# Kernel optimization log

Measured on AMD Instinct MI355X. Metric: run time of the kernel, lower is better.

The kernel has to match this reference:

```python
import jax, jax.numpy as jnp
import numpy as np

B, N, FIN = 4, 4096, 128
H, U = 4, 32

def setup_inputs() -> dict:
    key = jax.random.key(0)
    k = jax.random.split(key, 6)
    x = jax.random.normal(k[0], (B, N, FIN), dtype=jnp.float32)
    adj = (jax.random.uniform(k[1], (B, N, N)) < 0.05).astype(jnp.float32)
    glorot = lambda kk, shape, fi, fo: jax.random.uniform(kk, shape, jnp.float32,
                                                          -np.sqrt(6.0/(fi+fo)), np.sqrt(6.0/(fi+fo)))
    W = glorot(k[2], (FIN, H*U), FIN, H*U)
    a_src = glorot(k[3], (H, U, 1), U, 1)
    a_dst = glorot(k[4], (H, U, 1), U, 1)
    bias = jnp.zeros((H*U,), dtype=jnp.float32)
    return {"x": x, "adj": adj, "W": W, "a_src": a_src, "a_dst": a_dst, "bias": bias}

def reference(x, adj, W, a_src, a_dst, bias):
    # inference mode: attention dropout is a no-op
    b, n, _ = x.shape
    h_heads, u = a_src.shape[0], a_src.shape[1]
    # add self-loops, clip to {0,1}
    adj = jnp.clip(adj + jnp.eye(n, dtype=adj.dtype)[None], 0.0, 1.0)
    h = (x @ W).reshape(b, n, h_heads, u).transpose(0, 2, 1, 3)      # [B,H,N,U]
    f1 = jnp.einsum('bhnu,hu->bhn', h, a_src[..., 0])                # [B,H,N]
    f2 = jnp.einsum('bhnu,hu->bhn', h, a_dst[..., 0])                # [B,H,N]
    e = f1[:, :, :, None] + f2[:, :, None, :]                        # [B,H,N,N]
    e = jnp.where(e > 0, e, 0.2 * e)                                 # LeakyReLU(0.2)
    e = jnp.where(adj[:, None] > 0.0, e, jnp.float32(-1e9))
    alpha = jax.nn.softmax(e, axis=-1)
    out = jnp.einsum('bhij,bhju->bhiu', alpha, h)                    # [B,H,N,U]
    out = out.transpose(0, 2, 1, 3).reshape(b, n, h_heads * u) + bias
    return jnp.where(out > 0, out, jnp.expm1(out))                   # ELU
```

## Files before the change

### kernel.cpp

```cpp
#include <hip/hip_runtime.h>
#include <math.h>

#define NB   4
#define NN   4096
#define FIN  128
#define FOUT 128
#define NH   4
#define UU   32

__device__ __forceinline__ unsigned short f2bf(float f) {
    unsigned u = __float_as_uint(f);
    u += 0x7fff + ((u >> 16) & 1);
    return (unsigned short)(u >> 16);
}

#define LBAR() asm volatile("s_waitcnt lgkmcnt(0)\n\ts_barrier" ::: "memory")

#define K1_ROWS 64
#define K1_RT   8
#define K1_CT   4
#define XPAD    132

__global__ __launch_bounds__(256) void k1_feat(
    const float* __restrict__ x, const float* __restrict__ W,
    const float* __restrict__ a_src, const float* __restrict__ a_dst,
    unsigned short* __restrict__ hbf, float* __restrict__ f1g, float* __restrict__ f2g)
{
    __shared__ __align__(16) float Wq[32 * FOUT];
    __shared__ __align__(16) float xs[K1_ROWS * XPAD];

    const int tid  = threadIdx.x;
    const int row0 = blockIdx.x * K1_ROWS;

    const float4* x4 = (const float4*)(x + (size_t)row0 * FIN);
    for (int idx = tid; idx < K1_ROWS * FIN / 4; idx += 256) {
        int r = idx >> 5, q = idx & 31;
        *(float4*)(xs + r * XPAD + q * 4) = x4[idx];
    }

    const int cg = tid & 31;
    const int rg = tid >> 5;
    float acc[K1_RT][K1_CT];
    #pragma unroll
    for (int rr = 0; rr < K1_RT; rr++)
        #pragma unroll
        for (int cc = 0; cc < K1_CT; cc++) acc[rr][cc] = 0.f;

    for (int kt = 0; kt < 4; kt++) {
        __syncthreads();
        for (int idx = tid; idx < 32 * FOUT / 4; idx += 256)
            ((float4*)Wq)[idx] = ((const float4*)W)[kt * 1024 + idx];
        __syncthreads();
        #pragma unroll
        for (int k4 = 0; k4 < 8; k4++) {
            const int kb = kt * 32 + k4 * 4;
            float4 xv[K1_RT];
            #pragma unroll
            for (int rr = 0; rr < K1_RT; rr++)
                xv[rr] = *(const float4*)(xs + (rg * K1_RT + rr) * XPAD + kb);
            #pragma unroll
            for (int kk = 0; kk < 4; kk++) {
                float wv[K1_CT];
                #pragma unroll
                for (int cc = 0; cc < K1_CT; cc++)
                    wv[cc] = Wq[(k4 * 4 + kk) * FOUT + cg + 32 * cc];
                #pragma unroll
                for (int rr = 0; rr < K1_RT; rr++) {
                    float xk = ((const float*)&xv[rr])[kk];
                    #pragma unroll
                    for (int cc = 0; cc < K1_CT; cc++)
                        acc[rr][cc] = fmaf(xk, wv[cc], acc[rr][cc]);
                }
            }
        }
    }
    __syncthreads();
    #pragma unroll
    for (int rr = 0; rr < K1_RT; rr++)
        #pragma unroll
        for (int cc = 0; cc < K1_CT; cc++)
            xs[(rg * K1_RT + rr) * XPAD + cg + 32 * cc] = acc[rr][cc];
    __syncthreads();

    unsigned short* hrow = hbf + (size_t)row0 * FOUT;
    for (int idx = tid; idx < K1_ROWS * FOUT / 8; idx += 256) {
        int r = idx >> 4, q = idx & 15;
        const float* src = xs + r * XPAD + q * 8;
        uint4 o;
        o.x = (unsigned)f2bf(src[0]) | ((unsigned)f2bf(src[1]) << 16);
        o.y = (unsigned)f2bf(src[2]) | ((unsigned)f2bf(src[3]) << 16);
        o.z = (unsigned)f2bf(src[4]) | ((unsigned)f2bf(src[5]) << 16);
        o.w = (unsigned)f2bf(src[6]) | ((unsigned)f2bf(src[7]) << 16);
        *(uint4*)(hrow + (size_t)r * FOUT + q * 8) = o;
    }

    for (int task = tid; task < K1_ROWS * NH * 2; task += 256) {
        int row = task >> 3;
        int head = (task >> 1) & 3;
        int which = task & 1;
        const float* av = which ? a_dst : a_src;
        float s = 0.f;
        #pragma unroll
        for (int u = 0; u < UU; u++)
            s += xs[row * XPAD + head * UU + u] * av[head * UU + u];
        float* dst = which ? f2g : f1g;
        dst[(size_t)(row0 + row) * NH + head] = s;
    }
}

#define CAP   512
#define PPART 132
#define RPB   8

__device__ __forceinline__ float lrelu(float e) { return e > 0.f ? e : 0.2f * e; }

__global__ __launch_bounds__(256, 4) void k2_gat(
    const float* __restrict__ adj, const unsigned short* __restrict__ hbf,
    const float* __restrict__ f1g, const float* __restrict__ f2g,
    const float* __restrict__ bias, float* __restrict__ out)
{
    const int p    = blockIdx.x;
    const int xcd  = p & 7;
    const int b    = xcd >> 1;
    const int l    = ((p >> 3) << 1) | (p & 1);
    const int tid  = threadIdx.x;
    const int lane = tid & 63;
    const int wv   = tid >> 6;

    __shared__ int    nbr[CAP];
    __shared__ __align__(16) float4 alpha4[CAP];
    __shared__ float  part[16][PPART];
    __shared__ __align__(16) float4 smax4[4];
    __shared__ float  wsum[16];
    __shared__ int    wcnt[4];

    const float4* f2b = (const float4*)(f2g + (size_t)b * NN * NH);
    const unsigned short* hbase = hbf + (size_t)b * NN * FOUT;
    const unsigned long long below = (1ull << lane) - 1ull;

    const int cq = tid & 15, kg = tid >> 4, hh = cq >> 2;
    const unsigned short* hb = hbase + cq * 8;
    const float bias_r = (tid < FOUT) ? bias[tid] : 0.f;

    int i = l;
    float4 v[4], vn[4], f1v, f1n;
    {
        const float4* arow = (const float4*)(adj + (size_t)(b * NN + i) * NN);
        #pragma unroll
        for (int it = 0; it < 4; it++) v[it] = arow[wv * 256 + it * 64 + lane];
        f1v = ((const float4*)f1g)[b * NN + i];
    }

    for (int t = 0; t < RPB; t++) {
        const int row = b * NN + i;

        int my_cnt = 0;
        #pragma unroll
        for (int it = 0; it < 4; it++) {
            const int jb = (wv * 256 + it * 64 + lane) << 2;
            my_cnt += __popcll(__ballot((v[it].x > 0.f) | (jb + 0 == i)));
            my_cnt += __popcll(__ballot((v[it].y > 0.f) | (jb + 1 == i)));
            my_cnt += __popcll(__ballot((v[it].z > 0.f) | (jb + 2 == i)));
            my_cnt += __popcll(__ballot((v[it].w > 0.f) | (jb + 3 == i)));
        }
        if (lane == 0) wcnt[wv] = my_cnt;
        LBAR();

        const int w0 = wcnt[0], w1 = wcnt[1], w2 = wcnt[2], w3 = wcnt[3];
        int run = (wv > 0 ? w0 : 0) + (wv > 1 ? w1 : 0) + (wv > 2 ? w2 : 0);
        const int total = w0 + w1 + w2 + w3;
        const int K = (total < CAP) ? total : CAP;

        #pragma unroll
        for (int it = 0; it < 4; it++) {
            const int jb = (wv * 256 + it * 64 + lane) << 2;
            const bool p0 = (v[it].x > 0.f) | (jb + 0 == i);
            const bool p1 = (v[it].y > 0.f) | (jb + 1 == i);
            const bool p2 = (v[it].z > 0.f) | (jb + 2 == i);
            const bool p3 = (v[it].w > 0.f) | (jb + 3 == i);
            unsigned long long m0 = __ballot(p0), m1 = __ballot(p1);
            unsigned long long m2 = __ballot(p2), m3 = __ballot(p3);
            int c0 = __popcll(m0), c1 = __popcll(m1), c2 = __popcll(m2), c3 = __popcll(m3);
            if (p0) { int s = run + __popcll(m0 & below);                if (s < CAP) nbr[s] = jb + 0; }
            if (p1) { int s = run + c0 + __popcll(m1 & below);           if (s < CAP) nbr[s] = jb + 1; }
            if (p2) { int s = run + c0 + c1 + __popcll(m2 & below);      if (s < CAP) nbr[s] = jb + 2; }
            if (p3) { int s = run + c0 + c1 + c2 + __popcll(m3 & below); if (s < CAP) nbr[s] = jb + 3; }
            run += c0 + c1 + c2 + c3;
        }

        if (t + 1 < RPB) {
            const int inext = i + 512;
            const float4* arowN = (const float4*)(adj + (size_t)(b * NN + inext) * NN);
            #pragma unroll
            for (int it = 0; it < 4; it++) vn[it] = arowN[wv * 256 + it * 64 + lane];
            f1n = ((const float4*)f1g)[b * NN + inext];
        }
        LBAR();

        float4 hmax = make_float4(-1e30f, -1e30f, -1e30f, -1e30f);
        for (int k = tid; k < K; k += 256) {
            int j = nbr[k];
            float4 f2v = f2b[j];
            float4 e;
            e.x = lrelu(f1v.x + f2v.x);
            e.y = lrelu(f1v.y + f2v.y);
            e.z = lrelu(f1v.z + f2v.z);
            e.w = lrelu(f1v.w + f2v.w);
            alpha4[k] = e;
            hmax.x = fmaxf(hmax.x, e.x); hmax.y = fmaxf(hmax.y, e.y);
            hmax.z = fmaxf(hmax.z, e.z); hmax.w = fmaxf(hmax.w, e.w);
        }
        #pragma unroll
        for (int off = 32; off > 0; off >>= 1) {
            hmax.x = fmaxf(hmax.x, __shfl_xor(hmax.x, off, 64));
            hmax.y = fmaxf(hmax.y, __shfl_xor(hmax.y, off, 64));
            hmax.z = fmaxf(hmax.z, __shfl_xor(hmax.z, off, 64));
            hmax.w = fmaxf(hmax.w, __shfl_xor(hmax.w, off, 64));
        }
        if (lane == 0) smax4[wv] = hmax;
        LBAR();

        float4 g0 = smax4[0], g1 = smax4[1], g2 = smax4[2], g3 = smax4[3];
        float4 gmax;
        gmax.x = fmaxf(fmaxf(g0.x, g1.x), fmaxf(g2.x, g3.x));
        gmax.y = fmaxf(fmaxf(g0.y, g1.y), fmaxf(g2.y, g3.y));
        gmax.z = fmaxf(fmaxf(g0.z, g1.z), fmaxf(g2.z, g3.z));
        gmax.w = fmaxf(fmaxf(g0.w, g1.w), fmaxf(g2.w, g3.w));
        float4 hsum = make_float4(0.f, 0.f, 0.f, 0.f);
        for (int k = tid; k < K; k += 256) {
            float4 e = alpha4[k];
            e.x = __expf(e.x - gmax.x);
            e.y = __expf(e.y - gmax.y);
            e.z = __expf(e.z - gmax.z);
            e.w = __expf(e.w - gmax.w);
            alpha4[k] = e;
            hsum.x += e.x; hsum.y += e.y; hsum.z += e.z; hsum.w += e.w;
        }
        #pragma unroll
        for (int off = 32; off > 0; off >>= 1) {
            hsum.x += __shfl_xor(hsum.x, off, 64);
            hsum.y += __shfl_xor(hsum.y, off, 64);
            hsum.z += __shfl_xor(hsum.z, off, 64);
            hsum.w += __shfl_xor(hsum.w, off, 64);
        }
        if (lane == 0) {
            wsum[wv * 4 + 0] = hsum.x; wsum[wv * 4 + 1] = hsum.y;
            wsum[wv * 4 + 2] = hsum.z; wsum[wv * 4 + 3] = hsum.w;
        }
        LBAR();

        const float* alpf = (const float*)alpha4;
        float acc[8];
        #pragma unroll
        for (int u = 0; u < 8; u++) acc[u] = 0.f;
        int k = kg;
        for (; k + 16 < K; k += 32) {
            int j0 = nbr[k], j1 = nbr[k + 16];
            float a0 = alpf[k * 4 + hh], a1 = alpf[(k + 16) * 4 + hh];
            uint4 u4a = *(const uint4*)(hb + (size_t)j0 * FOUT);
            uint4 u4b = *(const uint4*)(hb + (size_t)j1 * FOUT);
            const unsigned* u0 = (const unsigned*)&u4a;
            const unsigned* u1 = (const unsigned*)&u4b;
            #pragma unroll
            for (int u = 0; u < 4; u++) {
                acc[2*u]   = fmaf(a0, __uint_as_float(u0[u] << 16),         acc[2*u]);
                acc[2*u+1] = fmaf(a0, __uint_as_float(u0[u] & 0xffff0000u), acc[2*u+1]);
            }
            #pragma unroll
            for (int u = 0; u < 4; u++) {
                acc[2*u]   = fmaf(a1, __uint_as_float(u1[u] << 16),         acc[2*u]);
                acc[2*u+1] = fmaf(a1, __uint_as_float(u1[u] & 0xffff0000u), acc[2*u+1]);
            }
        }
        if (k < K) {
            int j0 = nbr[k];
            float a0 = alpf[k * 4 + hh];
            uint4 u4a = *(const uint4*)(hb + (size_t)j0 * FOUT);
            const unsigned* u0 = (const unsigned*)&u4a;
            #pragma unroll
            for (int u = 0; u < 4; u++) {
                acc[2*u]   = fmaf(a0, __uint_as_float(u0[u] << 16),         acc[2*u]);
                acc[2*u+1] = fmaf(a0, __uint_as_float(u0[u] & 0xffff0000u), acc[2*u+1]);
            }
        }
        *(float4*)&part[kg][cq * 8]     = *(float4*)&acc[0];
        *(float4*)&part[kg][cq * 8 + 4] = *(float4*)&acc[4];
        LBAR();

        if (tid < FOUT) {
            const int h = tid >> 5;
            float s = wsum[h] + wsum[4 + h] + wsum[8 + h] + wsum[12 + h];
            float o = 0.f;
            #pragma unroll
            for (int g = 0; g < 16; g++) o += part[g][tid];
            o = o / s + bias_r;
            o = o > 0.f ? o : expm1f(o);
            out[(size_t)row * FOUT + tid] = o;
        }
        LBAR();

        if (t + 1 < RPB) {
            #pragma unroll
            for (int it = 0; it < 4; it++) v[it] = vn[it];
            f1v = f1n;
            i += 512;
        }
    }
}

extern "C" void kernel_launch(void* const* d_in, const int* in_sizes, int n_in,
                              void* d_out, int out_size, void* d_ws, size_t ws_size,
                              hipStream_t stream) {
    const float* x     = (const float*)d_in[0];
    const float* adj   = (const float*)d_in[1];
    const float* W     = (const float*)d_in[2];
    const float* a_src = (const float*)d_in[3];
    const float* a_dst = (const float*)d_in[4];
    const float* bias  = (const float*)d_in[5];
    float* out = (float*)d_out;

    char* ws = (char*)d_ws;
    unsigned short* hbf = (unsigned short*)ws;
    float* f1g = (float*)(ws + (size_t)NB * NN * FOUT * 2);
    float* f2g = f1g + (size_t)NB * NN * NH;

    k1_feat<<<NB * NN / K1_ROWS, 256, 0, stream>>>(x, W, a_src, a_dst, hbf, f1g, f2g);
    k2_gat<<<NB * NN / RPB, 256, 0, stream>>>(adj, hbf, f1g, f2g, bias, out);
}
```

Measured before the change: 437.4 us.

## Move adjacency compaction into the feature kernel and run one row per block

Neighbor-list extraction from the dense adjacency now runs in extra blocks of the first kernel, one wavefront per row. Each row's compacted 16-bit index list and count go to workspace, so the adjacency streaming overlaps the x@W projection. The attention kernel then reads the compact list and processes a single row per block with 16384 blocks. The cost is an extra global write and read of the neighbor lists, and the loss of the prefetch pipelining that previously hid adjacency loads behind compute.

```diff
diff --git a/kernel.cpp b/kernel.cpp
--- a/kernel.cpp
+++ b/kernel.cpp
@@ -7,6 +7,7 @@
 #define FOUT 128
 #define NH   4
 #define UU   32
+#define CAP  512
 
 __device__ __forceinline__ unsigned short f2bf(float f) {
     unsigned u = __float_as_uint(f);
@@ -16,20 +17,59 @@
 
 #define LBAR() asm volatile("s_waitcnt lgkmcnt(0)\n\ts_barrier" ::: "memory")
 
+__device__ __forceinline__ float lrelu(float e) { return e > 0.f ? e : 0.2f * e; }
+
 #define K1_ROWS 64
 #define K1_RT   8
 #define K1_CT   4
 #define XPAD    132
-
-__global__ __launch_bounds__(256) void k1_feat(
+#define K1_BLOCKS 256
+
+__global__ __launch_bounds__(256) void k0_fused(
     const float* __restrict__ x, const float* __restrict__ W,
     const float* __restrict__ a_src, const float* __restrict__ a_dst,
-    unsigned short* __restrict__ hbf, float* __restrict__ f1g, float* __restrict__ f2g)
+    const float* __restrict__ adj,
+    unsigned short* __restrict__ hbf, float* __restrict__ f1g, float* __restrict__ f2g,
+    unsigned short* __restrict__ nbr_g, int* __restrict__ kcnt)
 {
+    const int tid  = threadIdx.x;
+    const int lane = tid & 63;
+    const int wv   = tid >> 6;
+
     __shared__ __align__(16) float Wq[32 * FOUT];
     __shared__ __align__(16) float xs[K1_ROWS * XPAD];
 
-    const int tid  = threadIdx.x;
+    if (blockIdx.x >= K1_BLOCKS) {
+        const int r = (blockIdx.x - K1_BLOCKS) * 4 + wv;
+        const int i = r & (NN - 1);
+        const float4* arow = (const float4*)(adj + (size_t)r * NN);
+        float4 v[16];
+        #pragma unroll
+        for (int it = 0; it < 16; it++) v[it] = arow[it * 64 + lane];
+
+        unsigned short* ng = nbr_g + (size_t)r * CAP;
+        const unsigned long long below = (1ull << lane) - 1ull;
+        int run = 0;
+        #pragma unroll
+        for (int it = 0; it < 16; it++) {
+            const int jb = (it * 64 + lane) << 2;
+            const bool p0 = (v[it].x > 0.f) | (jb + 0 == i);
+            const bool p1 = (v[it].y > 0.f) | (jb + 1 == i);
+            const bool p2 = (v[it].z > 0.f) | (jb + 2 == i);
+            const bool p3 = (v[it].w > 0.f) | (jb + 3 == i);
+            unsigned long long m0 = __ballot(p0), m1 = __ballot(p1);
+            unsigned long long m2 = __ballot(p2), m3 = __ballot(p3);
+            int c0 = __popcll(m0), c1 = __popcll(m1), c2 = __popcll(m2), c3 = __popcll(m3);
+            if (p0) { int s = run + __popcll(m0 & below);                if (s < CAP) ng[s] = (unsigned short)(jb + 0); }
+            if (p1) { int s = run + c0 + __popcll(m1 & below);           if (s < CAP) ng[s] = (unsigned short)(jb + 1); }
+            if (p2) { int s = run + c0 + c1 + __popcll(m2 & below);      if (s < CAP) ng[s] = (unsigned short)(jb + 2); }
+            if (p3) { int s = run + c0 + c1 + c2 + __popcll(m3 & below); if (s < CAP) ng[s] = (unsigned short)(jb + 3); }
+            run += c0 + c1 + c2 + c3;
+        }
+        if (lane == 0) kcnt[r] = (run < CAP) ? run : CAP;
+        return;
+    }
+
     const int row0 = blockIdx.x * K1_ROWS;
 
     const float4* x4 = (const float4*)(x + (size_t)row0 * FIN);
@@ -60,16 +100,16 @@
                 xv[rr] = *(const float4*)(xs + (rg * K1_RT + rr) * XPAD + kb);
             #pragma unroll
             for (int kk = 0; kk < 4; kk++) {
-                float wv[K1_CT];
+                float wvv[K1_CT];
                 #pragma unroll
                 for (int cc = 0; cc < K1_CT; cc++)
-                    wv[cc] = Wq[(k4 * 4 + kk) * FOUT + cg + 32 * cc];
+                    wvv[cc] = Wq[(k4 * 4 + kk) * FOUT + cg + 32 * cc];
                 #pragma unroll
                 for (int rr = 0; rr < K1_RT; rr++) {
                     float xk = ((const float*)&xv[rr])[kk];
                     #pragma unroll
                     for (int cc = 0; cc < K1_CT; cc++)
-                        acc[rr][cc] = fmaf(xk, wv[cc], acc[rr][cc]);
+                        acc[rr][cc] = fmaf(xk, wvv[cc], acc[rr][cc]);
                 }
             }
         }
@@ -108,21 +148,19 @@
     }
 }
 
-#define CAP   512
 #define PPART 132
-#define RPB   8
-
-__device__ __forceinline__ float lrelu(float e) { return e > 0.f ? e : 0.2f * e; }
-
-__global__ __launch_bounds__(256, 4) void k2_gat(
-    const float* __restrict__ adj, const unsigned short* __restrict__ hbf,
+
+__global__ __launch_bounds__(256) void k2_gat(
+    const unsigned short* __restrict__ nbr_g, const int* __restrict__ kcnt,
+    const unsigned short* __restrict__ hbf,
     const float* __restrict__ f1g, const float* __restrict__ f2g,
     const float* __restrict__ bias, float* __restrict__ out)
 {
-    const int p    = blockIdx.x;
-    const int xcd  = p & 7;
+    const int q    = blockIdx.x;
+    const int xcd  = q & 7;
     const int b    = xcd >> 1;
-    const int l    = ((p >> 3) << 1) | (p & 1);
+    const int i    = ((q >> 3) << 1) | (q & 1);
+    const int row  = b * NN + i;
     const int tid  = threadIdx.x;
     const int lane = tid & 63;
     const int wv   = tid >> 6;
@@ -132,179 +170,117 @@
     __shared__ float  part[16][PPART];
     __shared__ __align__(16) float4 smax4[4];
     __shared__ float  wsum[16];
-    __shared__ int    wcnt[4];
+
+    const int K = kcnt[row];
+
+    const unsigned short* ng = nbr_g + (size_t)row * CAP;
+    for (int k = tid; k < K; k += 256) nbr[k] = (int)ng[k];
+    LBAR();
 
     const float4* f2b = (const float4*)(f2g + (size_t)b * NN * NH);
-    const unsigned short* hbase = hbf + (size_t)b * NN * FOUT;
-    const unsigned long long below = (1ull << lane) - 1ull;
+    const float4  f1v = ((const float4*)f1g)[row];
+
+    float4 hmax = make_float4(-1e30f, -1e30f, -1e30f, -1e30f);
+    for (int k = tid; k < K; k += 256) {
+        int j = nbr[k];
+        float4 f2v = f2b[j];
+        float4 e;
+        e.x = lrelu(f1v.x + f2v.x);
+        e.y = lrelu(f1v.y + f2v.y);
+        e.z = lrelu(f1v.z + f2v.z);
+        e.w = lrelu(f1v.w + f2v.w);
+        alpha4[k] = e;
+        hmax.x = fmaxf(hmax.x, e.x); hmax.y = fmaxf(hmax.y, e.y);
+        hmax.z = fmaxf(hmax.z, e.z); hmax.w = fmaxf(hmax.w, e.w);
+    }
+    #pragma unroll
+    for (int off = 32; off > 0; off >>= 1) {
+        hmax.x = fmaxf(hmax.x, __shfl_xor(hmax.x, off, 64));
+        hmax.y = fmaxf(hmax.y, __shfl_xor(hmax.y, off, 64));
+        hmax.z = fmaxf(hmax.z, __shfl_xor(hmax.z, off, 64));
+        hmax.w = fmaxf(hmax.w, __shfl_xor(hmax.w, off, 64));
+    }
+    if (lane == 0) smax4[wv] = hmax;
+    LBAR();
+
+    float4 g0 = smax4[0], g1 = smax4[1], g2 = smax4[2], g3 = smax4[3];
+    float4 gmax;
+    gmax.x = fmaxf(fmaxf(g0.x, g1.x), fmaxf(g2.x, g3.x));
+    gmax.y = fmaxf(fmaxf(g0.y, g1.y), fmaxf(g2.y, g3.y));
+    gmax.z = fmaxf(fmaxf(g0.z, g1.z), fmaxf(g2.z, g3.z));
+    gmax.w = fmaxf(fmaxf(g0.w, g1.w), fmaxf(g2.w, g3.w));
+    float4 hsum = make_float4(0.f, 0.f, 0.f, 0.f);
+    for (int k = tid; k < K; k += 256) {
+        float4 e = alpha4[k];
+        e.x = __expf(e.x - gmax.x);
+        e.y = __expf(e.y - gmax.y);
+        e.z = __expf(e.z - gmax.z);
+        e.w = __expf(e.w - gmax.w);
+        alpha4[k] = e;
+        hsum.x += e.x; hsum.y += e.y; hsum.z += e.z; hsum.w += e.w;
+    }
+    #pragma unroll
+    for (int off = 32; off > 0; off >>= 1) {
+        hsum.x += __shfl_xor(hsum.x, off, 64);
+        hsum.y += __shfl_xor(hsum.y, off, 64);
+        hsum.z += __shfl_xor(hsum.z, off, 64);
+        hsum.w += __shfl_xor(hsum.w, off, 64);
+    }
+    if (lane == 0) {
+        wsum[wv * 4 + 0] = hsum.x; wsum[wv * 4 + 1] = hsum.y;
+        wsum[wv * 4 + 2] = hsum.z; wsum[wv * 4 + 3] = hsum.w;
+    }
+    LBAR();
 
     const int cq = tid & 15, kg = tid >> 4, hh = cq >> 2;
-    const unsigned short* hb = hbase + cq * 8;
-    const float bias_r = (tid < FOUT) ? bias[tid] : 0.f;
-
-    int i = l;
-    float4 v[4], vn[4], f1v, f1n;
-    {
-        const float4* arow = (const float4*)(adj + (size_t)(b * NN + i) * NN);
-        #pragma unroll
-        for (int it = 0; it < 4; it++) v[it] = arow[wv * 256 + it * 64 + lane];
-        f1v = ((const float4*)f1g)[b * NN + i];
-    }
-
-    for (int t = 0; t < RPB; t++) {
-        const int row = b * NN + i;
-
-        int my_cnt = 0;
-        #pragma unroll
-        for (int it = 0; it < 4; it++) {
-            const int jb = (wv * 256 + it * 64 + lane) << 2;
-            my_cnt += __popcll(__ballot((v[it].x > 0.f) | (jb + 0 == i)));
-            my_cnt += __popcll(__ballot((v[it].y > 0.f) | (jb + 1 == i)));
-            my_cnt += __popcll(__ballot((v[it].z > 0.f) | (jb + 2 == i)));
-            my_cnt += __popcll(__ballot((v[it].w > 0.f) | (jb + 3 == i)));
-        }
-        if (lane == 0) wcnt[wv] = my_cnt;
-        LBAR();
-
-        const int w0 = wcnt[0], w1 = wcnt[1], w2 = wcnt[2], w3 = wcnt[3];
-        int run = (wv > 0 ? w0 : 0) + (wv > 1 ? w1 : 0) + (wv > 2 ? w2 : 0);
-        const int total = w0 + w1 + w2 + w3;
-        const int K = (total < CAP) ? total : CAP;
-
-        #pragma unroll
-        for (int it = 0; it < 4; it++) {
-            const int jb = (wv * 256 + it * 64 + lane) << 2;
-            const bool p0 = (v[it].x > 0.f) | (jb + 0 == i);
-            const bool p1 = (v[it].y > 0.f) | (jb + 1 == i);
-            const bool p2 = (v[it].z > 0.f) | (jb + 2 == i);
-            const bool p3 = (v[it].w > 0.f) | (jb + 3 == i);
-            unsigned long long m0 = __ballot(p0), m1 = __ballot(p1);
-            unsigned long long m2 = __ballot(p2), m3 = __ballot(p3);
-            int c0 = __popcll(m0), c1 = __popcll(m1), c2 = __popcll(m2), c3 = __popcll(m3);
-            if (p0) { int s = run + __popcll(m0 & below);                if (s < CAP) nbr[s] = jb + 0; }
-            if (p1) { int s = run + c0 + __popcll(m1 & below);           if (s < CAP) nbr[s] = jb + 1; }
-            if (p2) { int s = run + c0 + c1 + __popcll(m2 & below);      if (s < CAP) nbr[s] = jb + 2; }
-            if (p3) { int s = run + c0 + c1 + c2 + __popcll(m3 & below); if (s < CAP) nbr[s] = jb + 3; }
-            run += c0 + c1 + c2 + c3;
-        }
-
-        if (t + 1 < RPB) {
-            const int inext = i + 512;
-            const float4* arowN = (const float4*)(adj + (size_t)(b * NN + inext) * NN);
-            #pragma unroll
-            for (int it = 0; it < 4; it++) vn[it] = arowN[wv * 256 + it * 64 + lane];
-            f1n = ((const float4*)f1g)[b * NN + inext];
-        }
-        LBAR();
-
-        float4 hmax = make_float4(-1e30f, -1e30f, -1e30f, -1e30f);
-        for (int k = tid; k < K; k += 256) {
-            int j = nbr[k];
-            float4 f2v = f2b[j];
-            float4 e;
-            e.x = lrelu(f1v.x + f2v.x);
-            e.y = lrelu(f1v.y + f2v.y);
-            e.z = lrelu(f1v.z + f2v.z);
-            e.w = lrelu(f1v.w + f2v.w);
-            alpha4[k] = e;
-            hmax.x = fmaxf(hmax.x, e.x); hmax.y = fmaxf(hmax.y, e.y);
-            hmax.z = fmaxf(hmax.z, e.z); hmax.w = fmaxf(hmax.w, e.w);
-        }
-        #pragma unroll
-        for (int off = 32; off > 0; off >>= 1) {
-            hmax.x = fmaxf(hmax.x, __shfl_xor(hmax.x, off, 64));
-            hmax.y = fmaxf(hmax.y, __shfl_xor(hmax.y, off, 64));
-            hmax.z = fmaxf(hmax.z, __shfl_xor(hmax.z, off, 64));
-            hmax.w = fmaxf(hmax.w, __shfl_xor(hmax.w, off, 64));
-        }
-        if (lane == 0) smax4[wv] = hmax;
-        LBAR();
-
-        float4 g0 = smax4[0], g1 = smax4[1], g2 = smax4[2], g3 = smax4[3];
-        float4 gmax;
-        gmax.x = fmaxf(fmaxf(g0.x, g1.x), fmaxf(g2.x, g3.x));
-        gmax.y = fmaxf(fmaxf(g0.y, g1.y), fmaxf(g2.y, g3.y));
-        gmax.z = fmaxf(fmaxf(g0.z, g1.z), fmaxf(g2.z, g3.z));
-        gmax.w = fmaxf(fmaxf(g0.w, g1.w), fmaxf(g2.w, g3.w));
-        float4 hsum = make_float4(0.f, 0.f, 0.f, 0.f);
-        for (int k = tid; k < K; k += 256) {
-            float4 e = alpha4[k];
-            e.x = __expf(e.x - gmax.x);
-            e.y = __expf(e.y - gmax.y);
-            e.z = __expf(e.z - gmax.z);
-            e.w = __expf(e.w - gmax.w);
-            alpha4[k] = e;
-            hsum.x += e.x; hsum.y += e.y; hsum.z += e.z; hsum.w += e.w;
-        }
-        #pragma unroll
-        for (int off = 32; off > 0; off >>= 1) {
-            hsum.x += __shfl_xor(hsum.x, off, 64);
-            hsum.y += __shfl_xor(hsum.y, off, 64);
-            hsum.z += __shfl_xor(hsum.z, off, 64);
-            hsum.w += __shfl_xor(hsum.w, off, 64);
-        }
-        if (lane == 0) {
-            wsum[wv * 4 + 0] = hsum.x; wsum[wv * 4 + 1] = hsum.y;
-            wsum[wv * 4 + 2] = hsum.z; wsum[wv * 4 + 3] = hsum.w;
-        }
-        LBAR();
-
-        const float* alpf = (const float*)alpha4;
-        float acc[8];
-        #pragma unroll
-        for (int u = 0; u < 8; u++) acc[u] = 0.f;
-        int k = kg;
-        for (; k + 16 < K; k += 32) {
-            int j0 = nbr[k], j1 = nbr[k + 16];
-            float a0 = alpf[k * 4 + hh], a1 = alpf[(k + 16) * 4 + hh];
-            uint4 u4a = *(const uint4*)(hb + (size_t)j0 * FOUT);
-            uint4 u4b = *(const uint4*)(hb + (size_t)j1 * FOUT);
-            const unsigned* u0 = (const unsigned*)&u4a;
-            const unsigned* u1 = (const unsigned*)&u4b;
-            #pragma unroll
-            for (int u = 0; u < 4; u++) {
-                acc[2*u]   = fmaf(a0, __uint_as_float(u0[u] << 16),         acc[2*u]);
-                acc[2*u+1] = fmaf(a0, __uint_as_float(u0[u] & 0xffff0000u), acc[2*u+1]);
-            }
-            #pragma unroll
-            for (int u = 0; u < 4; u++) {
-                acc[2*u]   = fmaf(a1, __uint_as_float(u1[u] << 16),         acc[2*u]);
-                acc[2*u+1] = fmaf(a1, __uint_as_float(u1[u] & 0xffff0000u), acc[2*u+1]);
-            }
-        }
-        if (k < K) {
-            int j0 = nbr[k];
-            float a0 = alpf[k * 4 + hh];
-            uint4 u4a = *(const uint4*)(hb + (size_t)j0 * FOUT);
-            const unsigned* u0 = (const unsigned*)&u4a;
-            #pragma unroll
-            for (int u = 0; u < 4; u++) {
-                acc[2*u]   = fmaf(a0, __uint_as_float(u0[u] << 16),         acc[2*u]);
-                acc[2*u+1] = fmaf(a0, __uint_as_float(u0[u] & 0xffff0000u), acc[2*u+1]);
-            }
-        }
-        *(float4*)&part[kg][cq * 8]     = *(float4*)&acc[0];
-        *(float4*)&part[kg][cq * 8 + 4] = *(float4*)&acc[4];
-        LBAR();
-
-        if (tid < FOUT) {
-            const int h = tid >> 5;
-            float s = wsum[h] + wsum[4 + h] + wsum[8 + h] + wsum[12 + h];
-            float o = 0.f;
-            #pragma unroll
-            for (int g = 0; g < 16; g++) o += part[g][tid];
-            o = o / s + bias_r;
-            o = o > 0.f ? o : expm1f(o);
-            out[(size_t)row * FOUT + tid] = o;
-        }
-        LBAR();
-
-        if (t + 1 < RPB) {
-            #pragma unroll
-            for (int it = 0; it < 4; it++) v[it] = vn[it];
-            f1v = f1n;
-            i += 512;
-        }
+    const unsigned short* hb = hbf + (size_t)b * NN * FOUT + cq * 8;
+    const float* alpf = (const float*)alpha4;
+    float acc[8];
+    #pragma unroll
+    for (int u = 0; u < 8; u++) acc[u] = 0.f;
+    int k = kg;
+    for (; k + 16 < K; k += 32) {
+        int j0 = nbr[k], j1 = nbr[k + 16];
+        float a0 = alpf[k * 4 + hh], a1 = alpf[(k + 16) * 4 + hh];
+        uint4 u4a = *(const uint4*)(hb + (size_t)j0 * FOUT);
+        uint4 u4b = *(const uint4*)(hb + (size_t)j1 * FOUT);
+        const unsigned* u0 = (const unsigned*)&u4a;
+        const unsigned* u1 = (const unsigned*)&u4b;
+        #pragma unroll
+        for (int u = 0; u < 4; u++) {
+            acc[2*u]   = fmaf(a0, __uint_as_float(u0[u] << 16),         acc[2*u]);
+            acc[2*u+1] = fmaf(a0, __uint_as_float(u0[u] & 0xffff0000u), acc[2*u+1]);
+        }
+        #pragma unroll
+        for (int u = 0; u < 4; u++) {
+            acc[2*u]   = fmaf(a1, __uint_as_float(u1[u] << 16),         acc[2*u]);
+            acc[2*u+1] = fmaf(a1, __uint_as_float(u1[u] & 0xffff0000u), acc[2*u+1]);
+        }
+    }
+    if (k < K) {
+        int j0 = nbr[k];
+        float a0 = alpf[k * 4 + hh];
+        uint4 u4a = *(const uint4*)(hb + (size_t)j0 * FOUT);
+        const unsigned* u0 = (const unsigned*)&u4a;
+        #pragma unroll
+        for (int u = 0; u < 4; u++) {
+            acc[2*u]   = fmaf(a0, __uint_as_float(u0[u] << 16),         acc[2*u]);
+            acc[2*u+1] = fmaf(a0, __uint_as_float(u0[u] & 0xffff0000u), acc[2*u+1]);
+        }
+    }
+    *(float4*)&part[kg][cq * 8]     = *(float4*)&acc[0];
+    *(float4*)&part[kg][cq * 8 + 4] = *(float4*)&acc[4];
+    LBAR();
+
+    if (tid < FOUT) {
+        const int h = tid >> 5;
+        float s = wsum[h] + wsum[4 + h] + wsum[8 + h] + wsum[12 + h];
+        float o = 0.f;
+        #pragma unroll
+        for (int g = 0; g < 16; g++) o += part[g][tid];
+        o = o / s + bias[tid];
+        o = o > 0.f ? o : expm1f(o);
+        out[(size_t)row * FOUT + tid] = o;
     }
 }
 
@@ -320,10 +296,13 @@
     float* out = (float*)d_out;
 
     char* ws = (char*)d_ws;
-    unsigned short* hbf = (unsigned short*)ws;
-    float* f1g = (float*)(ws + (size_t)NB * NN * FOUT * 2);
-    float* f2g = f1g + (size_t)NB * NN * NH;
-
-    k1_feat<<<NB * NN / K1_ROWS, 256, 0, stream>>>(x, W, a_src, a_dst, hbf, f1g, f2g);
-    k2_gat<<<NB * NN / RPB, 256, 0, stream>>>(adj, hbf, f1g, f2g, bias, out);
+    unsigned short* hbf   = (unsigned short*)ws;
+    float*          f1g   = (float*)(ws + 4194304);
+    float*          f2g   = (float*)(ws + 4194304 + 262144);
+    unsigned short* nbr_g = (unsigned short*)(ws + 4194304 + 524288);
+    int*            kcnt  = (int*)(ws + 4194304 + 524288 + 16777216);
+
+    k0_fused<<<K1_BLOCKS + NB * NN / 4, 256, 0, stream>>>(
+        x, W, a_src, a_dst, adj, hbf, f1g, f2g, nbr_g, kcnt);
+    k2_gat<<<NB * NN, 256, 0, stream>>>(nbr_g, kcnt, hbf, f1g, f2g, bias, out);
 }
```

New measurement: 451.1 us. 1.03x slower.
